# Performance work log

Measured on AMD Instinct MI355X. Metric: run time of the kernel, lower is better.

The kernel has to match this reference:

```python
import jax, jax.numpy as jnp
import numpy as np

B, S, P, D, H, R = 2, 2048, 1024, 2048, 16, 16
DH = D // H  # 128


def _rope(t, cos, sin):
    # t: [B,S,H,DH]; cos/sin: [S, DH//2]; complex pair rotation
    t2 = t.reshape(t.shape[0], t.shape[1], t.shape[2], DH // 2, 2)
    a, b = t2[..., 0], t2[..., 1]
    c = cos[None, :, None, :]
    s = sin[None, :, None, :]
    out = jnp.stack([a * c - b * s, a * s + b * c], axis=-1)
    return out.reshape(t.shape)


def setup_inputs() -> dict:
    key = jax.random.key(0)
    ks = jax.random.split(key, 16)
    sc = 1.0 / np.sqrt(D)
    inv_freq = 1.0 / (10000.0 ** (np.arange(0, DH, 2, dtype=np.float32) / DH))
    pos = (P + np.arange(S, dtype=np.float32))[:, None] * inv_freq[None, :]
    i_idx = np.arange(S)[:, None]
    j_idx = np.arange(P + S)[None, :]
    mask = np.where(j_idx <= P + i_idx, 0.0, -1e9).astype(np.float32)
    return {
        "x": jax.random.normal(ks[0], (B, S, D), jnp.float32),
        "freqs_cos": jnp.asarray(np.cos(pos)),
        "freqs_sin": jnp.asarray(np.sin(pos)),
        "mask": jnp.asarray(mask)[None, None],
        "prev_key": jax.random.normal(ks[1], (B, P, H, DH), jnp.float32),
        "prev_value": jax.random.normal(ks[2], (B, P, H, DH), jnp.float32),
        "pooled_scale": jax.random.uniform(ks[3], (B, 1), jnp.float32),
        "wq": jax.random.normal(ks[4], (D, D), jnp.float32) * sc,
        "wk": jax.random.normal(ks[5], (D, D), jnp.float32) * sc,
        "wv": jax.random.normal(ks[6], (D, D), jnp.float32) * sc,
        "wo": jax.random.normal(ks[7], (D, D), jnp.float32) * sc,
        "wq_A": jax.random.normal(ks[8], (D, R), jnp.float32) * sc,
        "wq_B": jax.random.normal(ks[9], (R, D), jnp.float32) * 0.02,
        "wk_A": jax.random.normal(ks[10], (D, R), jnp.float32) * sc,
        "wk_B": jax.random.normal(ks[11], (R, D), jnp.float32) * 0.02,
        "wv_A": jax.random.normal(ks[12], (D, R), jnp.float32) * sc,
        "wv_B": jax.random.normal(ks[13], (R, D), jnp.float32) * 0.02,
        "wo_A": jax.random.normal(ks[14], (D, R), jnp.float32) * sc,
        "wo_B": jax.random.normal(ks[15], (R, D), jnp.float32) * 0.02,
    }


def reference(x, freqs_cos, freqs_sin, mask, prev_key, prev_value, pooled_scale,
              wq, wk, wv, wo, wq_A, wq_B, wk_A, wk_B, wv_A, wv_B, wo_A, wo_B):
    ps = pooled_scale[:, None, :]  # [B,1,1] per-batch LoRA scale
    xq = x @ wq.T + (x @ wq_A) @ wq_B * ps
    xk = x @ wk.T + (x @ wk_A) @ wk_B * ps
    xv = x @ wv.T + (x @ wv_A) @ wv_B * ps
    xq = xq.reshape(B, S, H, DH)
    xk = xk.reshape(B, S, H, DH)
    xv = xv.reshape(B, S, H, DH)
    xq = _rope(xq, freqs_cos, freqs_sin)
    xk = _rope(xk, freqs_cos, freqs_sin)
    keys = jnp.concatenate([prev_key, xk], axis=1)      # [B,P+S,H,DH]
    values = jnp.concatenate([prev_value, xv], axis=1)
    q = xq.transpose(0, 2, 1, 3)       # [B,H,S,DH]
    k = keys.transpose(0, 2, 1, 3)     # [B,H,P+S,DH]
    v = values.transpose(0, 2, 1, 3)
    scores = jnp.einsum("bhqd,bhkd->bhqk", q, k) / jnp.sqrt(jnp.float32(DH))
    scores = scores + mask
    probs = jax.nn.softmax(scores.astype(jnp.float32), axis=-1).astype(q.dtype)
    out = jnp.einsum("bhqk,bhkd->bhqd", probs, v)
    out = out.transpose(0, 2, 1, 3).reshape(B, S, D)
    return out @ wo.T + (out @ wo_A) @ wo_B * ps
```

## Files before the change

kernel.cpp:

```cpp
#include <hip/hip_runtime.h>
#include <stdint.h>

#define BB 2
#define SS 2048
#define PP 1024
#define DD 2048
#define HH 16
#define RR 16
#define DHH 128
#define TT (PP + SS)
#define BSR (BB * SS)

typedef __attribute__((ext_vector_type(8))) _Float16 half8;
typedef __attribute__((ext_vector_type(4))) float f32x4;

typedef __attribute__((address_space(3))) unsigned int lds_uint;
typedef const __attribute__((address_space(1))) unsigned int glb_uint;
__device__ __forceinline__ void async_copy16(const void* g, void* l) {
    __builtin_amdgcn_global_load_lds((glb_uint*)g, (lds_uint*)l, 16, 0, 0);
}

__global__ __launch_bounds__(256) void cvt_f16_kernel(
    const float* __restrict__ in, _Float16* __restrict__ out, int n4)
{
    int idx = blockIdx.x * 256 + threadIdx.x;
    int stride = gridDim.x * 256;
    for (int c = idx; c < n4; c += stride) {
        float4 v = *(const float4*)(in + (size_t)c * 4);
        union { _Float16 h[4]; uint2 u; } o;
        o.h[0] = (_Float16)v.x; o.h[1] = (_Float16)v.y;
        o.h[2] = (_Float16)v.z; o.h[3] = (_Float16)v.w;
        *(uint2*)(out + (size_t)c * 4) = o.u;
    }
}

__global__ __launch_bounds__(256) void lora_t_kernel(
    const float* __restrict__ A,
    const float* __restrict__ w0, const float* __restrict__ w1,
    const float* __restrict__ w2,
    float* __restrict__ tout)
{
    const float* wA = (blockIdx.z == 0) ? w0 : (blockIdx.z == 1) ? w1 : w2;
    int i  = blockIdx.x * 16 + (threadIdx.x >> 4);
    int r  = threadIdx.x & 15;
    int k0 = blockIdx.y * 512;
    const float* arow = A  + (size_t)i  * DD + k0;
    const float* wcol = wA + (size_t)k0 * RR + r;
    float acc = 0.f;
#pragma unroll 4
    for (int k = 0; k < 512; ++k)
        acc += arow[k] * wcol[k * RR];
    atomicAdd(&tout[(size_t)blockIdx.z * (BSR * RR) + (size_t)i * RR + r], acc);
}

__global__ __launch_bounds__(256) void lora_t_f16_kernel(
    const _Float16* __restrict__ A, const float* __restrict__ wA,
    float* __restrict__ tout)
{
    int i  = blockIdx.x * 16 + (threadIdx.x >> 4);
    int r  = threadIdx.x & 15;
    int k0 = blockIdx.y * 512;
    const _Float16* arow = A + (size_t)i * DD + k0;
    const float* wcol = wA + (size_t)k0 * RR + r;
    float acc = 0.f;
#pragma unroll 4
    for (int k = 0; k < 512; ++k)
        acc += (float)arow[k] * wcol[k * RR];
    atomicAdd(&tout[(size_t)i * RR + r], acc);
}

__global__ __launch_bounds__(256, 3) void gemm_f16_kernel(
    const _Float16* __restrict__ Ah, const _Float16* __restrict__ Wh,
    float* __restrict__ o0, float* __restrict__ o1, float* __restrict__ o2)
{
    __shared__ __align__(16) _Float16 As[128 * 32];
    __shared__ __align__(16) _Float16 Bs[128 * 32];
    const int tid  = threadIdx.x;
    const int wv   = tid >> 6;
    const int lane = tid & 63;
    const int ln   = lane & 15;
    const int quad = lane >> 4;
    const int i0   = blockIdx.x * 128;
    const int j0f  = blockIdx.y * 128;
    const int mat  = j0f >> 11;
    const int jloc = j0f & 2047;
    float* out_f = (mat == 0) ? o0 : (mat == 1) ? o1 : o2;
    const int mb   = (wv >> 1) * 4;
    const int nb   = (wv & 1) * 4;
    const int srow = wv * 32 + (lane >> 2);
    const int scol = (lane & 3) * 8;

    f32x4 zero = {0.f, 0.f, 0.f, 0.f};
    f32x4 acc[4][4];
#pragma unroll
    for (int a = 0; a < 4; ++a)
#pragma unroll
        for (int c = 0; c < 4; ++c) acc[a][c] = zero;

    const _Float16* gA = Ah + (size_t)(i0 + srow) * DD + scol;
    const _Float16* gB = Wh + (size_t)(j0f + srow) * DD + scol;
    _Float16* lA0 = As + (wv * 32) * 32;
    _Float16* lA1 = As + (wv * 32 + 16) * 32;
    _Float16* lB0 = Bs + (wv * 32) * 32;
    _Float16* lB1 = Bs + (wv * 32 + 16) * 32;

    for (int k0 = 0; k0 < DD; k0 += 32) {
        async_copy16(gA + k0, lA0);
        async_copy16(gA + (size_t)16 * DD + k0, lA1);
        async_copy16(gB + k0, lB0);
        async_copy16(gB + (size_t)16 * DD + k0, lB1);
        __syncthreads();
        half8 b[4];
#pragma unroll
        for (int nt = 0; nt < 4; ++nt)
            b[nt] = *(const half8*)&Bs[((nb + nt) * 16 + ln) * 32 + quad * 8];
#pragma unroll
        for (int mt = 0; mt < 4; ++mt) {
            half8 a = *(const half8*)&As[((mb + mt) * 16 + ln) * 32 + quad * 8];
#pragma unroll
            for (int nt = 0; nt < 4; ++nt)
                acc[mt][nt] = __builtin_amdgcn_mfma_f32_16x16x32_f16(a, b[nt], acc[mt][nt], 0, 0, 0);
        }
        __syncthreads();
    }

#pragma unroll
    for (int mt = 0; mt < 4; ++mt)
#pragma unroll
        for (int nt = 0; nt < 4; ++nt)
#pragma unroll
            for (int reg = 0; reg < 4; ++reg) {
                int row = i0 + (mb + mt) * 16 + quad * 4 + reg;
                int col = jloc + (nb + nt) * 16 + ln;
                out_f[(size_t)row * DD + col] = acc[mt][nt][reg];
            }
}

__global__ __launch_bounds__(256) void lora_add_kernel(
    const float* __restrict__ t, const float* __restrict__ wB,
    const float* __restrict__ ps, float* __restrict__ out)
{
    const int n4 = BSR * (DD / 4);
    int idx = blockIdx.x * 256 + threadIdx.x;
    int stride = gridDim.x * 256;
    for (int c = idx; c < n4; c += stride) {
        int i  = c >> 9;
        int j4 = c & 511;
        float psb = ps[i >> 11];
        const float* trow = t + (size_t)i * RR;
        float* op = out + (size_t)i * DD + j4 * 4;
        f32x4 acc = *(const f32x4*)op;
#pragma unroll
        for (int r = 0; r < 16; ++r) {
            float tv = psb * trow[r];
            f32x4 w = *(const f32x4*)(wB + (size_t)r * DD + j4 * 4);
#pragma unroll
            for (int q = 0; q < 4; ++q)
                acc[q] += tv * w[q];
        }
        *(f32x4*)op = acc;
    }
}

__global__ __launch_bounds__(256) void prev_scatter_kernel(
    const float* __restrict__ pk, const float* __restrict__ pv,
    _Float16* __restrict__ kh, _Float16* __restrict__ vTh)
{
    __shared__ __align__(16) _Float16 vt[128][72];
    const int pt = blockIdx.x, h = blockIdx.y;
    const int b = pt >> 4, p0 = (pt & 15) * 64;
    const int tid = threadIdx.x;
    const size_t bh = (size_t)(b * HH + h);
#pragma unroll
    for (int p = 0; p < 8; ++p) {
        int c = tid + 256 * p;
        int pl = c >> 5, c4 = (c & 31) * 4;
        float4 v4 = *(const float4*)(pk + (((size_t)(b * PP + p0 + pl)) * HH + h) * DHH + c4);
        union { _Float16 h4[4]; uint2 u; } o;
        o.h4[0] = (_Float16)v4.x; o.h4[1] = (_Float16)v4.y;
        o.h4[2] = (_Float16)v4.z; o.h4[3] = (_Float16)v4.w;
        *(uint2*)(kh + (bh * TT + p0 + pl) * DHH + c4) = o.u;
    }
#pragma unroll
    for (int p = 0; p < 8; ++p) {
        int c = tid + 256 * p;
        int pl = c >> 5, c4 = (c & 31) * 4;
        float4 v4 = *(const float4*)(pv + (((size_t)(b * PP + p0 + pl)) * HH + h) * DHH + c4);
        vt[c4 + 0][pl] = (_Float16)v4.x;
        vt[c4 + 1][pl] = (_Float16)v4.y;
        vt[c4 + 2][pl] = (_Float16)v4.z;
        vt[c4 + 3][pl] = (_Float16)v4.w;
    }
    __syncthreads();
#pragma unroll
    for (int p = 0; p < 4; ++p) {
        int c = tid + 256 * p;
        int d = c >> 3, c8 = (c & 7) * 8;
        *(half8*)(vTh + (bh * DHH + d) * TT + p0 + c8) = *(const half8*)&vt[d][c8];
    }
}

__global__ __launch_bounds__(256) void rope_scatter_kernel(
    const float* __restrict__ xq, const float* __restrict__ xk,
    const float* __restrict__ xv,
    const float* __restrict__ t_all,
    const float* __restrict__ wqB, const float* __restrict__ wkB,
    const float* __restrict__ wvB,
    const float* __restrict__ ps,
    const float* __restrict__ fcos, const float* __restrict__ fsin,
    _Float16* __restrict__ qh, _Float16* __restrict__ kh,
    _Float16* __restrict__ vTh)
{
    __shared__ float tS[64][48];
    __shared__ float wBs[3][16][128];
    __shared__ __align__(16) _Float16 vt[128][72];
    const int st = blockIdx.x, h = blockIdx.y;
    const int i0 = st * 64;
    const int b  = i0 >> 11;
    const int s0 = i0 & 2047;
    const int tid = threadIdx.x;
    const size_t bh = (size_t)(b * HH + h);
    const float QSC = 0.12753102f;

#pragma unroll
    for (int p = 0; p < 12; ++p) {
        int idx = tid + 256 * p;
        int w = idx >> 10, rem = idx & 1023;
        int sl = rem >> 4, r = rem & 15;
        tS[sl][w * 16 + r] = t_all[(size_t)w * (BSR * RR) + (size_t)(i0 + sl) * RR + r];
    }
#pragma unroll
    for (int w = 0; w < 3; ++w) {
        const float* src = (w == 0) ? wqB : (w == 1) ? wkB : wvB;
#pragma unroll
        for (int p = 0; p < 8; ++p) {
            int idx = tid + 256 * p;
            int r = idx >> 7, dd = idx & 127;
            wBs[w][r][dd] = src[(size_t)r * DD + h * DHH + dd];
        }
    }
    __syncthreads();
    const float psb = ps[b];

#pragma unroll
    for (int w = 0; w < 2; ++w) {
        const float* src = (w == 0) ? xq : xk;
        for (int p = 0; p < 16; ++p) {
            int pp = tid + 256 * p;
            int sl = pp >> 6, dd = pp & 63;
            int d = dd * 2;
            int i = i0 + sl, s = s0 + sl;
            float2 pr = *(const float2*)(src + (size_t)i * DD + h * DHH + d);
            float a = pr.x, b2 = pr.y;
            float la = 0.f, lb = 0.f;
#pragma unroll
            for (int r = 0; r < 16; ++r) {
                float tv = tS[sl][w * 16 + r];
                la += tv * wBs[w][r][d];
                lb += tv * wBs[w][r][d + 1];
            }
            a  += psb * la;
            b2 += psb * lb;
            float c  = fcos[(size_t)s * 64 + dd];
            float sn = fsin[(size_t)s * 64 + dd];
            float na = a * c - b2 * sn;
            float nb = a * sn + b2 * c;
            union { _Float16 h2[2]; unsigned u; } o;
            if (w == 0) {
                o.h2[0] = (_Float16)(na * QSC); o.h2[1] = (_Float16)(nb * QSC);
                *(unsigned*)(qh + (bh * SS + s) * DHH + d) = o.u;
            } else {
                o.h2[0] = (_Float16)na; o.h2[1] = (_Float16)nb;
                *(unsigned*)(kh + (bh * TT + PP + s) * DHH + d) = o.u;
            }
        }
    }
    for (int p = 0; p < 16; ++p) {
        int pp = tid + 256 * p;
        int sl = pp >> 6, dd = pp & 63;
        int d = dd * 2;
        int i = i0 + sl;
        float2 pr = *(const float2*)(xv + (size_t)i * DD + h * DHH + d);
        float a = pr.x, b2 = pr.y;
        float la = 0.f, lb = 0.f;
#pragma unroll
        for (int r = 0; r < 16; ++r) {
            float tv = tS[sl][32 + r];
            la += tv * wBs[2][r][d];
            lb += tv * wBs[2][r][d + 1];
        }
        a  += psb * la;
        b2 += psb * lb;
        vt[d][sl]     = (_Float16)a;
        vt[d + 1][sl] = (_Float16)b2;
    }
    __syncthreads();
#pragma unroll
    for (int p = 0; p < 4; ++p) {
        int c = tid + 256 * p;
        int d = c >> 3, c8 = (c & 7) * 8;
        *(half8*)(vTh + (bh * DHH + d) * TT + PP + s0 + c8) = *(const half8*)&vt[d][c8];
    }
}

__global__ __launch_bounds__(256) void attn_kernel(
    const _Float16* __restrict__ qh, const _Float16* __restrict__ kh,
    const _Float16* __restrict__ vTh, _Float16* __restrict__ attn_h)
{
    __shared__ __align__(16) _Float16 k_lds[64][136];
    __shared__ __align__(16) _Float16 v_lds[128][72];
    __shared__ __align__(16) _Float16 p_lds[4][2][16][72];
    const int lin = blockIdx.x;
    int bh_i, qt;
    if (lin < 256) { bh_i = lin & 31; qt = lin >> 5; }
    else { int l2 = lin - 256; bh_i = l2 & 31; qt = 15 - (l2 >> 5); }
    const int h = bh_i & 15, b = bh_i >> 4;
    const int qbase = qt * 128;
    const int tid = threadIdx.x, wv = tid >> 6, lane = tid & 63;
    const int ln = lane & 15, quad = lane >> 4;
    const size_t bh = (size_t)(b * HH + h);

    half8 qfrag[2][4];
#pragma unroll
    for (int mt = 0; mt < 2; ++mt) {
        const _Float16* qrow = qh + (bh * SS + qbase + wv * 32 + mt * 16 + ln) * DHH;
#pragma unroll
        for (int ks = 0; ks < 4; ++ks)
            qfrag[mt][ks] = *(const half8*)(qrow + ks * 32 + quad * 8);
    }
    f32x4 zero = {0.f, 0.f, 0.f, 0.f};
    f32x4 O[2][8];
#pragma unroll
    for (int mt = 0; mt < 2; ++mt)
#pragma unroll
        for (int i = 0; i < 8; ++i) O[mt][i] = zero;
    float l_part[2][4];
#pragma unroll
    for (int mt = 0; mt < 2; ++mt)
#pragma unroll
        for (int r = 0; r < 4; ++r) l_part[mt][r] = 0.f;

    int offKg[4], offKl[4], offVg[4], offVl[4];
#pragma unroll
    for (int p = 0; p < 4; ++p) {
        int c = tid + 256 * p;
        int key = c >> 4, ck = (c & 15) * 8;
        offKg[p] = key * DHH + ck;
        offKl[p] = key * 136 + ck;
        int d = c >> 3, cv = (c & 7) * 8;
        offVg[p] = d * TT + cv;
        offVl[p] = d * 72 + cv;
    }
    const _Float16* kbase = kh + bh * (size_t)TT * DHH;
    const _Float16* vbase = vTh + bh * (size_t)DHH * TT;

    const int ntiles = 18 + 2 * qt;

    half8 k0r[4], v0r[4], k1r[4], v1r[4];
#pragma unroll
    for (int p = 0; p < 4; ++p) {
        k0r[p] = *(const half8*)(kbase + offKg[p]);
        v0r[p] = *(const half8*)(vbase + offVg[p]);
    }

#define ATTN_BODY(KT, KC, VC, KN, VN)                                          \
  {                                                                            \
    const int kb = (KT) * 64;                                                  \
    _Pragma("unroll")                                                          \
    for (int p = 0; p < 4; ++p) {                                              \
        *(half8*)((_Float16*)k_lds + offKl[p]) = KC[p];                        \
        *(half8*)((_Float16*)v_lds + offVl[p]) = VC[p];                        \
    }                                                                          \
    __syncthreads();                                                           \
    if ((KT) + 1 < ntiles) {                                                   \
        const _Float16* kg = kbase + (size_t)(kb + 64) * DHH;                  \
        const _Float16* vg = vbase + (kb + 64);                                \
        _Pragma("unroll")                                                      \
        for (int p = 0; p < 4; ++p) {                                          \
            KN[p] = *(const half8*)(kg + offKg[p]);                            \
            VN[p] = *(const half8*)(vg + offVg[p]);                            \
        }                                                                      \
    }                                                                          \
    f32x4 sv[2][4];                                                            \
    __builtin_amdgcn_s_setprio(1);                                             \
    _Pragma("unroll")                                                          \
    for (int nt = 0; nt < 4; ++nt) {                                           \
        half8 kf[4];                                                           \
        _Pragma("unroll")                                                      \
        for (int ks = 0; ks < 4; ++ks)                                         \
            kf[ks] = *(const half8*)&k_lds[nt * 16 + ln][ks * 32 + quad * 8];  \
        _Pragma("unroll")                                                      \
        for (int mt = 0; mt < 2; ++mt) {                                       \
            f32x4 s = zero;                                                    \
            _Pragma("unroll")                                                  \
            for (int ks = 0; ks < 4; ++ks)                                     \
                s = __builtin_amdgcn_mfma_f32_16x16x32_f16(qfrag[mt][ks], kf[ks], s, 0, 0, 0); \
            sv[mt][nt] = s;                                                    \
        }                                                                      \
    }                                                                          \
    __builtin_amdgcn_s_setprio(0);                                             \
    const bool tail = ((KT) >= ntiles - 2);                                    \
    _Pragma("unroll")                                                          \
    for (int mt = 0; mt < 2; ++mt)                                             \
        _Pragma("unroll")                                                      \
        for (int nt = 0; nt < 4; ++nt)                                         \
            _Pragma("unroll")                                                  \
            for (int reg = 0; reg < 4; ++reg) {                                \
                float z = sv[mt][nt][reg];                                     \
                if (tail) {                                                    \
                    int jj = kb + nt * 16 + ln;                                \
                    int rg = PP + qbase + wv * 32 + mt * 16 + quad * 4 + reg;  \
                    if (jj > rg) z = -1e30f;                                   \
                }                                                              \
                float pz = exp2f(z - 12.f);                                    \
                l_part[mt][reg] += pz;                                         \
                {                                                              \
                    int row = quad * 4 + reg;                                  \
                    int cs  = (nt * 2 + (ln >> 3)) ^ ((row >> 1) & 7);         \
                    p_lds[wv][mt][row][cs * 8 + (ln & 7)] = (_Float16)pz;      \
                }                                                              \
            }                                                                  \
    __builtin_amdgcn_s_setprio(1);                                             \
    _Pragma("unroll")                                                          \
    for (int kf2 = 0; kf2 < 2; ++kf2) {                                        \
        int cA = ((kf2 * 4 + quad) ^ ((ln >> 1) & 7)) * 8;                     \
        half8 pa0 = *(const half8*)&p_lds[wv][0][ln][cA];                      \
        half8 pa1 = *(const half8*)&p_lds[wv][1][ln][cA];                      \
        _Pragma("unroll")                                                      \
        for (int d8 = 0; d8 < 8; ++d8) {                                       \
            half8 vb = *(const half8*)&v_lds[d8 * 16 + ln][kf2 * 32 + quad * 8]; \
            O[0][d8] = __builtin_amdgcn_mfma_f32_16x16x32_f16(pa0, vb, O[0][d8], 0, 0, 0); \
            O[1][d8] = __builtin_amdgcn_mfma_f32_16x16x32_f16(pa1, vb, O[1][d8], 0, 0, 0); \
        }                                                                      \
    }                                                                          \
    __builtin_amdgcn_s_setprio(0);                                             \
    __syncthreads();                                                           \
  }

    for (int kt = 0; kt < ntiles; kt += 2) {
        ATTN_BODY(kt,     k0r, v0r, k1r, v1r);
        ATTN_BODY(kt + 1, k1r, v1r, k0r, v0r);
    }
#undef ATTN_BODY

#pragma unroll
    for (int mt = 0; mt < 2; ++mt)
#pragma unroll
        for (int reg = 0; reg < 4; ++reg) {
            float l = l_part[mt][reg];
#pragma unroll
            for (int off = 1; off < 16; off <<= 1)
                l += __shfl_xor(l, off);
            l_part[mt][reg] = 1.f / l;
        }
#pragma unroll
    for (int mt = 0; mt < 2; ++mt)
#pragma unroll
        for (int d8 = 0; d8 < 8; ++d8)
#pragma unroll
            for (int reg = 0; reg < 4; ++reg) {
                int row = qbase + wv * 32 + mt * 16 + quad * 4 + reg;
                int col = h * DHH + d8 * 16 + ln;
                attn_h[((size_t)b * SS + row) * DD + col] =
                    (_Float16)(O[mt][d8][reg] * l_part[mt][reg]);
            }
}

extern "C" void kernel_launch(void* const* d_in, const int* in_sizes, int n_in,
                              void* d_out, int out_size, void* d_ws, size_t ws_size,
                              hipStream_t stream) {
    const float* x    = (const float*)d_in[0];
    const float* fcos = (const float*)d_in[1];
    const float* fsin = (const float*)d_in[2];
    const float* pk   = (const float*)d_in[4];
    const float* pv   = (const float*)d_in[5];
    const float* ps   = (const float*)d_in[6];
    const float* wq   = (const float*)d_in[7];
    const float* wk   = (const float*)d_in[8];
    const float* wvw  = (const float*)d_in[9];
    const float* wo   = (const float*)d_in[10];
    const float* wqA  = (const float*)d_in[11];
    const float* wqB  = (const float*)d_in[12];
    const float* wkA  = (const float*)d_in[13];
    const float* wkB  = (const float*)d_in[14];
    const float* wvA  = (const float*)d_in[15];
    const float* wvB  = (const float*)d_in[16];
    const float* woA  = (const float*)d_in[17];
    const float* woB  = (const float*)d_in[18];
    float* out = (float*)d_out;

    float* t_all = (float*)d_ws;
    float* t_o   = t_all + 3 * BSR * RR;
    float* xq    = t_all + 4 * BSR * RR;
    float* xk    = xq + (size_t)BSR * DD;
    float* xv    = xk + (size_t)BSR * DD;
    _Float16* xh    = (_Float16*)(xv + (size_t)BSR * DD);
    _Float16* wqkvh = xh + (size_t)BSR * DD;
    _Float16* woh   = wqkvh + (size_t)3 * DD * DD;
    _Float16* qh_   = woh + (size_t)DD * DD;
    _Float16* kh_   = qh_ + (size_t)BB * HH * SS * DHH;
    _Float16* vTh   = kh_ + (size_t)BB * HH * TT * DHH;
    _Float16* attn_h = vTh + (size_t)BB * HH * DHH * TT;
    (void)ws_size; (void)in_sizes; (void)n_in; (void)out_size;

    hipMemsetAsync(t_all, 0, (size_t)4 * BSR * RR * sizeof(float), stream);

    cvt_f16_kernel<<<512, 256, 0, stream>>>(x,   xh, (BSR * DD) / 4);
    cvt_f16_kernel<<<512, 256, 0, stream>>>(wq,  wqkvh,                       (DD * DD) / 4);
    cvt_f16_kernel<<<512, 256, 0, stream>>>(wk,  wqkvh + (size_t)DD * DD,     (DD * DD) / 4);
    cvt_f16_kernel<<<512, 256, 0, stream>>>(wvw, wqkvh + (size_t)2 * DD * DD, (DD * DD) / 4);
    cvt_f16_kernel<<<512, 256, 0, stream>>>(wo,  woh, (DD * DD) / 4);

    lora_t_kernel<<<dim3(256, 4, 3), 256, 0, stream>>>(x, wqA, wkA, wvA, t_all);

    gemm_f16_kernel<<<dim3(32, 48), 256, 0, stream>>>(xh, wqkvh, xq, xk, xv);

    prev_scatter_kernel<<<dim3(32, 16), 256, 0, stream>>>(pk, pv, kh_, vTh);

    rope_scatter_kernel<<<dim3(64, 16), 256, 0, stream>>>(xq, xk, xv, t_all,
                                                          wqB, wkB, wvB, ps,
                                                          fcos, fsin,
                                                          qh_, kh_, vTh);

    attn_kernel<<<512, 256, 0, stream>>>(qh_, kh_, vTh, attn_h);

    lora_t_f16_kernel<<<dim3(256, 4), 256, 0, stream>>>(attn_h, woA, t_o);

    gemm_f16_kernel<<<dim3(32, 16), 256, 0, stream>>>(attn_h, woh, out, out, out);

    lora_add_kernel<<<2048, 256, 0, stream>>>(t_o, woB, ps, out);
}
```

Before: 766.0 us.

## Split long causal attention query tiles across two blocks with partial-sum combine

The attention grid now splits the heavier query tiles (upper half) into two key-range chunks, each computed by a separate block, giving 768 blocks instead of 512. Partial unnormalized outputs and row sums go to scratch buffers reusing the xq/xk workspace, and a new combine kernel sums them and normalizes into attn_h. This relies on the fixed exp2 offset (no running max), so partial results add directly. It aims to balance the work per block and improve CU utilization, at the cost of extra fp32 traffic and one more launch.

```diff
diff --git a/kernel.cpp b/kernel.cpp
--- a/kernel.cpp
+++ b/kernel.cpp
@@ -305,16 +305,27 @@
 
 __global__ __launch_bounds__(256) void attn_kernel(
     const _Float16* __restrict__ qh, const _Float16* __restrict__ kh,
-    const _Float16* __restrict__ vTh, _Float16* __restrict__ attn_h)
+    const _Float16* __restrict__ vTh, _Float16* __restrict__ attn_h,
+    float* __restrict__ pbuf, float* __restrict__ lbuf)
 {
     __shared__ __align__(16) _Float16 k_lds[64][136];
     __shared__ __align__(16) _Float16 v_lds[128][72];
     __shared__ __align__(16) _Float16 p_lds[4][2][16][72];
     const int lin = blockIdx.x;
-    int bh_i, qt;
-    if (lin < 256) { bh_i = lin & 31; qt = lin >> 5; }
-    else { int l2 = lin - 256; bh_i = l2 & 31; qt = 15 - (l2 >> 5); }
+    const int cblk = lin & 255;
+    const int s    = lin >> 8;
+    const int q8   = cblk & 7;
+    const int bh_i = cblk >> 3;
     const int h = bh_i & 15, b = bh_i >> 4;
+    int qt, t0, t1, ntf;
+    if (s == 0) { qt = q8;      ntf = 18 + 2 * q8; t0 = 0; t1 = ntf; }
+    else {
+        qt = 15 - q8; ntf = 48 - 2 * q8;
+        int mid = (24 - q8) & ~1;
+        if (s == 1) { t0 = 0;   t1 = mid; }
+        else        { t0 = mid; t1 = ntf; }
+    }
+    const bool partial = (s != 0);
     const int qbase = qt * 128;
     const int tid = threadIdx.x, wv = tid >> 6, lane = tid & 63;
     const int ln = lane & 15, quad = lane >> 4;
@@ -354,13 +365,15 @@
     const _Float16* kbase = kh + bh * (size_t)TT * DHH;
     const _Float16* vbase = vTh + bh * (size_t)DHH * TT;
 
-    const int ntiles = 18 + 2 * qt;
-
     half8 k0r[4], v0r[4], k1r[4], v1r[4];
-#pragma unroll
-    for (int p = 0; p < 4; ++p) {
-        k0r[p] = *(const half8*)(kbase + offKg[p]);
-        v0r[p] = *(const half8*)(vbase + offVg[p]);
+    {
+        const _Float16* kg0 = kbase + (size_t)(t0 * 64) * DHH;
+        const _Float16* vg0 = vbase + t0 * 64;
+#pragma unroll
+        for (int p = 0; p < 4; ++p) {
+            k0r[p] = *(const half8*)(kg0 + offKg[p]);
+            v0r[p] = *(const half8*)(vg0 + offVg[p]);
+        }
     }
 
 #define ATTN_BODY(KT, KC, VC, KN, VN)                                          \
@@ -372,7 +385,7 @@
         *(half8*)((_Float16*)v_lds + offVl[p]) = VC[p];                        \
     }                                                                          \
     __syncthreads();                                                           \
-    if ((KT) + 1 < ntiles) {                                                   \
+    if ((KT) + 1 < t1) {                                                       \
         const _Float16* kg = kbase + (size_t)(kb + 64) * DHH;                  \
         const _Float16* vg = vbase + (kb + 64);                                \
         _Pragma("unroll")                                                      \
@@ -391,15 +404,15 @@
             kf[ks] = *(const half8*)&k_lds[nt * 16 + ln][ks * 32 + quad * 8];  \
         _Pragma("unroll")                                                      \
         for (int mt = 0; mt < 2; ++mt) {                                       \
-            f32x4 s = zero;                                                    \
+            f32x4 sacc = zero;                                                 \
             _Pragma("unroll")                                                  \
             for (int ks = 0; ks < 4; ++ks)                                     \
-                s = __builtin_amdgcn_mfma_f32_16x16x32_f16(qfrag[mt][ks], kf[ks], s, 0, 0, 0); \
-            sv[mt][nt] = s;                                                    \
+                sacc = __builtin_amdgcn_mfma_f32_16x16x32_f16(qfrag[mt][ks], kf[ks], sacc, 0, 0, 0); \
+            sv[mt][nt] = sacc;                                                 \
         }                                                                      \
     }                                                                          \
     __builtin_amdgcn_s_setprio(0);                                             \
-    const bool tail = ((KT) >= ntiles - 2);                                    \
+    const bool tail = ((KT) >= ntf - 2);                                       \
     _Pragma("unroll")                                                          \
     for (int mt = 0; mt < 2; ++mt)                                             \
         _Pragma("unroll")                                                      \
@@ -437,7 +450,7 @@
     __syncthreads();                                                           \
   }
 
-    for (int kt = 0; kt < ntiles; kt += 2) {
+    for (int kt = t0; kt < t1; kt += 2) {
         ATTN_BODY(kt,     k0r, v0r, k1r, v1r);
         ATTN_BODY(kt + 1, k1r, v1r, k0r, v0r);
     }
@@ -451,19 +464,69 @@
 #pragma unroll
             for (int off = 1; off < 16; off <<= 1)
                 l += __shfl_xor(l, off);
-            l_part[mt][reg] = 1.f / l;
-        }
-#pragma unroll
-    for (int mt = 0; mt < 2; ++mt)
-#pragma unroll
-        for (int d8 = 0; d8 < 8; ++d8)
-#pragma unroll
-            for (int reg = 0; reg < 4; ++reg) {
-                int row = qbase + wv * 32 + mt * 16 + quad * 4 + reg;
-                int col = h * DHH + d8 * 16 + ln;
-                attn_h[((size_t)b * SS + row) * DD + col] =
-                    (_Float16)(O[mt][d8][reg] * l_part[mt][reg]);
-            }
+            l_part[mt][reg] = l;
+        }
+
+    if (!partial) {
+#pragma unroll
+        for (int mt = 0; mt < 2; ++mt)
+#pragma unroll
+            for (int d8 = 0; d8 < 8; ++d8)
+#pragma unroll
+                for (int reg = 0; reg < 4; ++reg) {
+                    int row = qbase + wv * 32 + mt * 16 + quad * 4 + reg;
+                    int col = h * DHH + d8 * 16 + ln;
+                    attn_h[((size_t)b * SS + row) * DD + col] =
+                        (_Float16)(O[mt][d8][reg] / l_part[mt][reg]);
+                }
+    } else {
+        const int chunkid = cblk * 2 + (s - 1);
+        float* pb = pbuf + (size_t)chunkid * (128 * 128);
+        float* lb = lbuf + (size_t)chunkid * 128;
+#pragma unroll
+        for (int mt = 0; mt < 2; ++mt)
+#pragma unroll
+            for (int reg = 0; reg < 4; ++reg)
+                if (ln == 0)
+                    lb[wv * 32 + mt * 16 + quad * 4 + reg] = l_part[mt][reg];
+#pragma unroll
+        for (int mt = 0; mt < 2; ++mt)
+#pragma unroll
+            for (int d8 = 0; d8 < 8; ++d8)
+#pragma unroll
+                for (int reg = 0; reg < 4; ++reg) {
+                    int row = wv * 32 + mt * 16 + quad * 4 + reg;
+                    pb[(size_t)row * 128 + d8 * 16 + ln] = O[mt][d8][reg];
+                }
+    }
+}
+
+__global__ __launch_bounds__(256) void attn_combine_kernel(
+    const float* __restrict__ pbuf, const float* __restrict__ lbuf,
+    _Float16* __restrict__ attn_h)
+{
+    const int cblk = blockIdx.x;
+    const int q8 = cblk & 7, bh_i = cblk >> 3;
+    const int h = bh_i & 15, b = bh_i >> 4;
+    const int qt = 15 - q8, qbase = qt * 128;
+    const int tid = threadIdx.x;
+    const int row = tid >> 1, c0 = (tid & 1) * 64;
+    const float* pa = pbuf + (size_t)(cblk * 2) * (128 * 128) + (size_t)row * 128 + c0;
+    const float* pbv = pa + 128 * 128;
+    float inv = 1.f / (lbuf[(size_t)(cblk * 2) * 128 + row] +
+                       lbuf[(size_t)(cblk * 2 + 1) * 128 + row]);
+    _Float16* orow = attn_h + ((size_t)b * SS + qbase + row) * DD + h * DHH + c0;
+#pragma unroll
+    for (int j = 0; j < 64; j += 4) {
+        float4 va = *(const float4*)(pa + j);
+        float4 vb = *(const float4*)(pbv + j);
+        union { _Float16 h4[4]; uint2 u; } o;
+        o.h4[0] = (_Float16)((va.x + vb.x) * inv);
+        o.h4[1] = (_Float16)((va.y + vb.y) * inv);
+        o.h4[2] = (_Float16)((va.z + vb.z) * inv);
+        o.h4[3] = (_Float16)((va.w + vb.w) * inv);
+        *(uint2*)(orow + j) = o.u;
+    }
 }
 
 extern "C" void kernel_launch(void* const* d_in, const int* in_sizes, int n_in,
@@ -501,6 +564,8 @@
     _Float16* kh_   = qh_ + (size_t)BB * HH * SS * DHH;
     _Float16* vTh   = kh_ + (size_t)BB * HH * TT * DHH;
     _Float16* attn_h = vTh + (size_t)BB * HH * DHH * TT;
+    float* pbuf = xq;
+    float* lbuf = xk;
     (void)ws_size; (void)in_sizes; (void)n_in; (void)out_size;
 
     hipMemsetAsync(t_all, 0, (size_t)4 * BSR * RR * sizeof(float), stream);
@@ -522,7 +587,9 @@
                                                           fcos, fsin,
                                                           qh_, kh_, vTh);
 
-    attn_kernel<<<512, 256, 0, stream>>>(qh_, kh_, vTh, attn_h);
+    attn_kernel<<<768, 256, 0, stream>>>(qh_, kh_, vTh, attn_h, pbuf, lbuf);
+
+    attn_combine_kernel<<<256, 256, 0, stream>>>(pbuf, lbuf, attn_h);
 
     lora_t_f16_kernel<<<dim3(256, 4), 256, 0, stream>>>(attn_h, woA, t_o);
 
```

Result: slower. 786.7 us (+2.7%).

## Halve attention query tile to 64 rows and merge five f16 conversion launches

Applied to the files above, without the earlier changes.

The attention kernel now gives each block 64 query rows instead of 128, with one 16-row MMA tile per wave. This doubles the grid to 1024 blocks, shrinks causal waste on the diagonal tile, and lowers register and LDS pressure for better occupancy. The cost is that each K/V tile loaded into LDS is reused by half as many queries, so global K/V traffic doubles. The five separate fp32-to-fp16 conversion launches are also merged into one 2D-grid launch to cut launch overhead.

```diff
diff --git a/kernel.cpp b/kernel.cpp
--- a/kernel.cpp
+++ b/kernel.cpp
@@ -20,9 +20,24 @@
     __builtin_amdgcn_global_load_lds((glb_uint*)g, (lds_uint*)l, 16, 0, 0);
 }
 
-__global__ __launch_bounds__(256) void cvt_f16_kernel(
-    const float* __restrict__ in, _Float16* __restrict__ out, int n4)
-{
+__global__ __launch_bounds__(256) void cvt_f16x5_kernel(
+    const float* __restrict__ s0, const float* __restrict__ s1,
+    const float* __restrict__ s2, const float* __restrict__ s3,
+    const float* __restrict__ s4,
+    _Float16* __restrict__ dx, _Float16* __restrict__ dqkv,
+    _Float16* __restrict__ dwo)
+{
+    const int seg = blockIdx.y;
+    const float* in;
+    _Float16* out;
+    int n4;
+    if (seg == 0)      { in = s0; out = dx;  n4 = (BSR * DD) / 4; }
+    else if (seg == 4) { in = s4; out = dwo; n4 = (DD * DD) / 4; }
+    else {
+        in  = (seg == 1) ? s1 : (seg == 2) ? s2 : s3;
+        out = dqkv + (size_t)(seg - 1) * DD * DD;
+        n4  = (DD * DD) / 4;
+    }
     int idx = blockIdx.x * 256 + threadIdx.x;
     int stride = gridDim.x * 256;
     for (int c = idx; c < n4; c += stride) {
@@ -309,36 +324,32 @@
 {
     __shared__ __align__(16) _Float16 k_lds[64][136];
     __shared__ __align__(16) _Float16 v_lds[128][72];
-    __shared__ __align__(16) _Float16 p_lds[4][2][16][72];
+    __shared__ __align__(16) _Float16 p_lds[4][16][72];
     const int lin = blockIdx.x;
-    int bh_i, qt;
-    if (lin < 256) { bh_i = lin & 31; qt = lin >> 5; }
-    else { int l2 = lin - 256; bh_i = l2 & 31; qt = 15 - (l2 >> 5); }
+    const int bh_i = lin & 31;
+    const int t5   = lin >> 5;
+    const int qtp  = (lin < 512) ? t5 : 47 - t5;
     const int h = bh_i & 15, b = bh_i >> 4;
-    const int qbase = qt * 128;
+    const int qbase = qtp * 64;
+    const int ntiles = 17 + qtp;
     const int tid = threadIdx.x, wv = tid >> 6, lane = tid & 63;
     const int ln = lane & 15, quad = lane >> 4;
     const size_t bh = (size_t)(b * HH + h);
 
-    half8 qfrag[2][4];
-#pragma unroll
-    for (int mt = 0; mt < 2; ++mt) {
-        const _Float16* qrow = qh + (bh * SS + qbase + wv * 32 + mt * 16 + ln) * DHH;
+    half8 qfrag[4];
+    {
+        const _Float16* qrow = qh + (bh * SS + qbase + wv * 16 + ln) * DHH;
 #pragma unroll
         for (int ks = 0; ks < 4; ++ks)
-            qfrag[mt][ks] = *(const half8*)(qrow + ks * 32 + quad * 8);
+            qfrag[ks] = *(const half8*)(qrow + ks * 32 + quad * 8);
     }
     f32x4 zero = {0.f, 0.f, 0.f, 0.f};
-    f32x4 O[2][8];
-#pragma unroll
-    for (int mt = 0; mt < 2; ++mt)
-#pragma unroll
-        for (int i = 0; i < 8; ++i) O[mt][i] = zero;
-    float l_part[2][4];
-#pragma unroll
-    for (int mt = 0; mt < 2; ++mt)
-#pragma unroll
-        for (int r = 0; r < 4; ++r) l_part[mt][r] = 0.f;
+    f32x4 O[8];
+#pragma unroll
+    for (int i = 0; i < 8; ++i) O[i] = zero;
+    float l_part[4];
+#pragma unroll
+    for (int r = 0; r < 4; ++r) l_part[r] = 0.f;
 
     int offKg[4], offKl[4], offVg[4], offVl[4];
 #pragma unroll
@@ -353,8 +364,6 @@
     }
     const _Float16* kbase = kh + bh * (size_t)TT * DHH;
     const _Float16* vbase = vTh + bh * (size_t)DHH * TT;
-
-    const int ntiles = 18 + 2 * qt;
 
     half8 k0r[4], v0r[4], k1r[4], v1r[4];
 #pragma unroll
@@ -381,7 +390,7 @@
             VN[p] = *(const half8*)(vg + offVg[p]);                            \
         }                                                                      \
     }                                                                          \
-    f32x4 sv[2][4];                                                            \
+    f32x4 sv[4];                                                               \
     __builtin_amdgcn_s_setprio(1);                                             \
     _Pragma("unroll")                                                          \
     for (int nt = 0; nt < 4; ++nt) {                                           \
@@ -389,81 +398,78 @@
         _Pragma("unroll")                                                      \
         for (int ks = 0; ks < 4; ++ks)                                         \
             kf[ks] = *(const half8*)&k_lds[nt * 16 + ln][ks * 32 + quad * 8];  \
+        f32x4 sacc = zero;                                                     \
         _Pragma("unroll")                                                      \
-        for (int mt = 0; mt < 2; ++mt) {                                       \
-            f32x4 s = zero;                                                    \
-            _Pragma("unroll")                                                  \
-            for (int ks = 0; ks < 4; ++ks)                                     \
-                s = __builtin_amdgcn_mfma_f32_16x16x32_f16(qfrag[mt][ks], kf[ks], s, 0, 0, 0); \
-            sv[mt][nt] = s;                                                    \
-        }                                                                      \
+        for (int ks = 0; ks < 4; ++ks)                                         \
+            sacc = __builtin_amdgcn_mfma_f32_16x16x32_f16(qfrag[ks], kf[ks], sacc, 0, 0, 0); \
+        sv[nt] = sacc;                                                         \
     }                                                                          \
     __builtin_amdgcn_s_setprio(0);                                             \
-    const bool tail = ((KT) >= ntiles - 2);                                    \
+    const bool tail = ((KT) == ntiles - 1);                                    \
     _Pragma("unroll")                                                          \
-    for (int mt = 0; mt < 2; ++mt)                                             \
+    for (int nt = 0; nt < 4; ++nt)                                             \
         _Pragma("unroll")                                                      \
-        for (int nt = 0; nt < 4; ++nt)                                         \
-            _Pragma("unroll")                                                  \
-            for (int reg = 0; reg < 4; ++reg) {                                \
-                float z = sv[mt][nt][reg];                                     \
-                if (tail) {                                                    \
-                    int jj = kb + nt * 16 + ln;                                \
-                    int rg = PP + qbase + wv * 32 + mt * 16 + quad * 4 + reg;  \
-                    if (jj > rg) z = -1e30f;                                   \
-                }                                                              \
-                float pz = exp2f(z - 12.f);                                    \
-                l_part[mt][reg] += pz;                                         \
-                {                                                              \
-                    int row = quad * 4 + reg;                                  \
-                    int cs  = (nt * 2 + (ln >> 3)) ^ ((row >> 1) & 7);         \
-                    p_lds[wv][mt][row][cs * 8 + (ln & 7)] = (_Float16)pz;      \
-                }                                                              \
+        for (int reg = 0; reg < 4; ++reg) {                                    \
+            float z = sv[nt][reg];                                             \
+            if (tail) {                                                        \
+                int jj = nt * 16 + ln;                                         \
+                int rg = wv * 16 + quad * 4 + reg;                             \
+                if (jj > rg) z = -1e30f;                                       \
             }                                                                  \
+            float pz = exp2f(z - 12.f);                                        \
+            l_part[reg] += pz;                                                 \
+            {                                                                  \
+                int row = quad * 4 + reg;                                      \
+                int cs  = (nt * 2 + (ln >> 3)) ^ ((row >> 1) & 7);             \
+                p_lds[wv][row][cs * 8 + (ln & 7)] = (_Float16)pz;              \
+            }                                                                  \
+        }                                                                      \
     __builtin_amdgcn_s_setprio(1);                                             \
     _Pragma("unroll")                                                          \
     for (int kf2 = 0; kf2 < 2; ++kf2) {                                        \
         int cA = ((kf2 * 4 + quad) ^ ((ln >> 1) & 7)) * 8;                     \
-        half8 pa0 = *(const half8*)&p_lds[wv][0][ln][cA];                      \
-        half8 pa1 = *(const half8*)&p_lds[wv][1][ln][cA];                      \
+        half8 pa = *(const half8*)&p_lds[wv][ln][cA];                          \
         _Pragma("unroll")                                                      \
         for (int d8 = 0; d8 < 8; ++d8) {                                       \
             half8 vb = *(const half8*)&v_lds[d8 * 16 + ln][kf2 * 32 + quad * 8]; \
-            O[0][d8] = __builtin_amdgcn_mfma_f32_16x16x32_f16(pa0, vb, O[0][d8], 0, 0, 0); \
-            O[1][d8] = __builtin_amdgcn_mfma_f32_16x16x32_f16(pa1, vb, O[1][d8], 0, 0, 0); \
+            O[d8] = __builtin_amdgcn_mfma_f32_16x16x32_f16(pa, vb, O[d8], 0, 0, 0); \
         }                                                                      \
     }                                                                          \
     __builtin_amdgcn_s_setprio(0);                                             \
     __syncthreads();                                                           \
   }
 
-    for (int kt = 0; kt < ntiles; kt += 2) {
-        ATTN_BODY(kt,     k0r, v0r, k1r, v1r);
-        ATTN_BODY(kt + 1, k1r, v1r, k0r, v0r);
+    if (ntiles & 1) {
+        ATTN_BODY(0, k0r, v0r, k1r, v1r);
+        for (int kt = 1; kt < ntiles; kt += 2) {
+            ATTN_BODY(kt,     k1r, v1r, k0r, v0r);
+            ATTN_BODY(kt + 1, k0r, v0r, k1r, v1r);
+        }
+    } else {
+        for (int kt = 0; kt < ntiles; kt += 2) {
+            ATTN_BODY(kt,     k0r, v0r, k1r, v1r);
+            ATTN_BODY(kt + 1, k1r, v1r, k0r, v0r);
+        }
     }
 #undef ATTN_BODY
 
 #pragma unroll
-    for (int mt = 0; mt < 2; ++mt)
+    for (int reg = 0; reg < 4; ++reg) {
+        float l = l_part[reg];
+#pragma unroll
+        for (int off = 1; off < 16; off <<= 1)
+            l += __shfl_xor(l, off);
+        l_part[reg] = 1.f / l;
+    }
+#pragma unroll
+    for (int d8 = 0; d8 < 8; ++d8)
 #pragma unroll
         for (int reg = 0; reg < 4; ++reg) {
-            float l = l_part[mt][reg];
-#pragma unroll
-            for (int off = 1; off < 16; off <<= 1)
-                l += __shfl_xor(l, off);
-            l_part[mt][reg] = 1.f / l;
-        }
-#pragma unroll
-    for (int mt = 0; mt < 2; ++mt)
-#pragma unroll
-        for (int d8 = 0; d8 < 8; ++d8)
-#pragma unroll
-            for (int reg = 0; reg < 4; ++reg) {
-                int row = qbase + wv * 32 + mt * 16 + quad * 4 + reg;
-                int col = h * DHH + d8 * 16 + ln;
-                attn_h[((size_t)b * SS + row) * DD + col] =
-                    (_Float16)(O[mt][d8][reg] * l_part[mt][reg]);
-            }
+            int row = qbase + wv * 16 + quad * 4 + reg;
+            int col = h * DHH + d8 * 16 + ln;
+            attn_h[((size_t)b * SS + row) * DD + col] =
+                (_Float16)(O[d8][reg] * l_part[reg]);
+        }
 }
 
 extern "C" void kernel_launch(void* const* d_in, const int* in_sizes, int n_in,
@@ -505,11 +511,8 @@
 
     hipMemsetAsync(t_all, 0, (size_t)4 * BSR * RR * sizeof(float), stream);
 
-    cvt_f16_kernel<<<512, 256, 0, stream>>>(x,   xh, (BSR * DD) / 4);
-    cvt_f16_kernel<<<512, 256, 0, stream>>>(wq,  wqkvh,                       (DD * DD) / 4);
-    cvt_f16_kernel<<<512, 256, 0, stream>>>(wk,  wqkvh + (size_t)DD * DD,     (DD * DD) / 4);
-    cvt_f16_kernel<<<512, 256, 0, stream>>>(wvw, wqkvh + (size_t)2 * DD * DD, (DD * DD) / 4);
-    cvt_f16_kernel<<<512, 256, 0, stream>>>(wo,  woh, (DD * DD) / 4);
+    cvt_f16x5_kernel<<<dim3(512, 5), 256, 0, stream>>>(x, wq, wk, wvw, wo,
+                                                       xh, wqkvh, woh);
 
     lora_t_kernel<<<dim3(256, 4, 3), 256, 0, stream>>>(x, wqA, wkA, wvA, t_all);
 
@@ -522,7 +525,7 @@
                                                           fcos, fsin,
                                                           qh_, kh_, vTh);
 
-    attn_kernel<<<512, 256, 0, stream>>>(qh_, kh_, vTh, attn_h);
+    attn_kernel<<<1024, 256, 0, stream>>>(qh_, kh_, vTh, attn_h);
 
     lora_t_f16_kernel<<<dim3(256, 4), 256, 0, stream>>>(attn_h, woA, t_o);
 
```

Result: no change. 752.8 us (-1.7%).
